# Optimization experiments

Measured on AMD Instinct MI355X. Metric: run time of the kernel, lower is better.

Reference implementation:

```python
import jax, jax.numpy as jnp
import numpy as np

B, Hs, Ws, DIM = 8, 32, 32, 768
NH, HD = 12, 64  # num_heads, head_dim


def get_rel_pos(size, rel_pos):
    # q_size == k_size == size; no interpolation branch needed
    coords = jnp.arange(size)[:, None] - jnp.arange(size)[None, :] + (size - 1)
    return rel_pos[coords]  # (size, size, head_dim)


def setup_inputs() -> dict:
    key = jax.random.key(0)
    ks = jax.random.split(key, 7)
    inv = 1.0 / np.sqrt(DIM)
    return {
        "x": jax.random.normal(ks[0], (B, Hs, Ws, DIM), jnp.float32),
        "qkv_w": jax.random.normal(ks[1], (3 * DIM, DIM), jnp.float32) * inv,
        "qkv_b": jax.random.normal(ks[2], (3 * DIM,), jnp.float32) * 0.02,
        "proj_w": jax.random.normal(ks[3], (DIM, DIM), jnp.float32) * inv,
        "proj_b": jax.random.normal(ks[4], (DIM,), jnp.float32) * 0.02,
        "rel_pos_h": jax.random.normal(ks[5], (2 * Hs - 1, HD), jnp.float32) * 0.02,
        "rel_pos_w": jax.random.normal(ks[6], (2 * Ws - 1, HD), jnp.float32) * 0.02,
    }


def reference(x, qkv_w, qkv_b, proj_w, proj_b, rel_pos_h, rel_pos_w):
    Bb, H, W, C = x.shape
    L = H * W
    scale = HD ** -0.5

    qkv = x @ qkv_w.T + qkv_b                       # (B,H,W,3C)
    qkv = qkv.reshape(Bb, L, 3, NH, HD).transpose(2, 0, 3, 1, 4)
    q, k, v = qkv[0], qkv[1], qkv[2]                # (B,NH,L,HD)

    # decomposed 2D relative position bias
    rel_h = get_rel_pos(H, rel_pos_h)               # (H,H,HD)
    rel_w = get_rel_pos(W, rel_pos_w)               # (W,W,HD)
    q5 = q.reshape(Bb, NH, H, W, HD)
    rel_h_attn = jnp.einsum('bnhwc,hkc->bnhwk', q5, rel_h)  # (B,NH,H,W,H)
    rel_w_attn = jnp.einsum('bnhwc,wkc->bnhwk', q5, rel_w)  # (B,NH,H,W,W)
    bias = rel_h_attn[..., :, None] + rel_w_attn[..., None, :]  # (B,NH,H,W,H,W)
    bias = bias.reshape(Bb, NH, L, L)

    scores = jnp.einsum('bnqd,bnkd->bnqk', q, k) * scale + bias
    attn = jax.nn.softmax(scores, axis=-1)
    out = jnp.einsum('bnqk,bnkd->bnqd', attn, v)    # (B,NH,L,HD)

    out = out.reshape(Bb, NH, H, W, HD).transpose(0, 2, 3, 1, 4).reshape(Bb, H, W, C)
    return out @ proj_w.T + proj_b
```

## Files before the change

kernel.cpp:

```cpp
#include <hip/hip_runtime.h>

typedef unsigned short u16;
typedef __bf16 bf16x8 __attribute__((ext_vector_type(8)));
typedef float f32x4 __attribute__((ext_vector_type(4)));

#define NHEAD 12
#define LQ 1024
#define HDIM 64
#define DIMM 768

__device__ __forceinline__ u16 f2b(float f) {
  unsigned u = __float_as_uint(f);
  u += 0x7fffu + ((u >> 16) & 1u);
  return (u16)(u >> 16);
}
__device__ __forceinline__ float b2f(u16 v) {
  return __uint_as_float(((unsigned)v) << 16);
}
__device__ __forceinline__ unsigned cvt_pk(float lo, float hi) {
  unsigned r;
  asm("v_cvt_pk_bf16_f32 %0, %1, %2" : "=v"(r) : "v"(lo), "v"(hi));
  return r;
}
__device__ __forceinline__ void async16(const void* g, void* l) {
  __builtin_amdgcn_global_load_lds(
      (const __attribute__((address_space(1))) void*)g,
      (__attribute__((address_space(3))) void*)l, 16, 0, 0);
}

__global__ __launch_bounds__(256) void cvt_kernel(const float* __restrict__ in,
                                                  u16* __restrict__ out, int n4) {
  int i = blockIdx.x * 256 + threadIdx.x;
  if (i >= n4) return;
  const float4 v = reinterpret_cast<const float4*>(in)[i];
  ushort4 o;
  o.x = f2b(v.x); o.y = f2b(v.y); o.z = f2b(v.z); o.w = f2b(v.w);
  reinterpret_cast<ushort4*>(out)[i] = o;
}

__global__ __launch_bounds__(256) void cvt_rel(const float* __restrict__ rph,
                                               const float* __restrict__ rpw,
                                               u16* __restrict__ rphb,
                                               u16* __restrict__ rpwb) {
  int i = blockIdx.x * 256 + threadIdx.x;
  int tab = i >> 12, idx = i & 4095;
  int m = idx >> 6, d = idx & 63;
  const float* src = tab ? rpw : rph;
  u16* dst = tab ? rpwb : rphb;
  dst[idx] = (m < 63) ? f2b(src[m * HDIM + d]) : (u16)0;
}

__global__ __launch_bounds__(256) void gemm_qkv(const u16* __restrict__ A,
                                                const u16* __restrict__ Bt,
                                                const float* __restrict__ bias,
                                                u16* __restrict__ qb,
                                                u16* __restrict__ kb,
                                                u16* __restrict__ vtb) {
  __shared__ u16 la[128 * 32];
  __shared__ u16 lb[128 * 32];
  const int K = DIMM;
  int t = threadIdx.x;
  int lane = t & 63, wv = t >> 6;
  int l15 = lane & 15, l4 = lane >> 4;
  int bm = blockIdx.x / 18, bn = blockIdx.x % 18;
  int m0 = bm * 128, n0 = bn * 128;
  int wm = (wv >> 1) * 64, wn = (wv & 1) * 64;

  f32x4 acc[4][4];
  #pragma unroll
  for (int i = 0; i < 4; ++i)
    #pragma unroll
    for (int j = 0; j < 4; ++j) acc[i][j] = {0.f, 0.f, 0.f, 0.f};

  for (int k0 = 0; k0 < K; k0 += 32) {
    __syncthreads();
    #pragma unroll
    for (int i = 0; i < 2; ++i) {
      int c = i * 256 + t;
      int row = c >> 2, co = c & 3;
      async16(A + (m0 + row) * K + k0 + co * 8, (char*)la + c * 16);
      async16(Bt + (n0 + row) * K + k0 + co * 8, (char*)lb + c * 16);
    }
    __syncthreads();
    bf16x8 af[4], bfr[4];
    #pragma unroll
    for (int mi = 0; mi < 4; ++mi)
      af[mi] = *reinterpret_cast<const bf16x8*>(&la[(wm + mi * 16 + l15) * 32 + l4 * 8]);
    #pragma unroll
    for (int nj = 0; nj < 4; ++nj)
      bfr[nj] = *reinterpret_cast<const bf16x8*>(&lb[(wn + nj * 16 + l15) * 32 + l4 * 8]);
    #pragma unroll
    for (int mi = 0; mi < 4; ++mi)
      #pragma unroll
      for (int nj = 0; nj < 4; ++nj)
        acc[mi][nj] = __builtin_amdgcn_mfma_f32_16x16x32_bf16(af[mi], bfr[nj], acc[mi][nj], 0, 0, 0);
  }

  int part = (n0 >> 7) / 6;
  #pragma unroll
  for (int nj = 0; nj < 4; ++nj) {
    int n = n0 + wn + nj * 16 + l15;
    float bv = bias[n];
    int d = n & 63;
    int head = (n >> 6) % NHEAD;
    #pragma unroll
    for (int mi = 0; mi < 4; ++mi) {
      #pragma unroll
      for (int r = 0; r < 4; ++r) {
        int m = m0 + wm + mi * 16 + l4 * 4 + r;
        int b = m >> 10, li = m & 1023;
        int bh = b * NHEAD + head;
        u16 o = f2b(acc[mi][nj][r] + bv);
        if (part == 0)      qb[(bh * LQ + li) * HDIM + d] = o;
        else if (part == 1) kb[(bh * LQ + li) * HDIM + d] = o;
        else                vtb[(bh * HDIM + d) * LQ + li] = o;
      }
    }
  }
}

__global__ __launch_bounds__(256) void attn_kernel(const u16* __restrict__ qb,
                                                   const u16* __restrict__ kb,
                                                   const u16* __restrict__ vtb,
                                                   const u16* __restrict__ rphb,
                                                   const u16* __restrict__ rpwb,
                                                   u16* __restrict__ ao) {
  __shared__ u16 lds_k[64 * 64];
  __shared__ u16 lds_v[64 * 64];
  __shared__ u16 lds_th[64 * 72];
  __shared__ u16 lds_tw[64 * 72];
  __shared__ u16 lds_p[4][16 * 72];

  int bid = blockIdx.x;
  int bh = bid >> 4;
  int q0 = (bid & 15) * 64;
  int t = threadIdx.x;
  int wv = t >> 6, lane = t & 63;
  int l15 = lane & 15, l4 = lane >> 4;

  bf16x8 qf[2];
  {
    const u16* qsrc = qb + (bh * LQ + q0 + wv * 16 + l15) * HDIM + l4 * 8;
    qf[0] = *reinterpret_cast<const bf16x8*>(qsrc);
    qf[1] = *reinterpret_cast<const bf16x8*>(qsrc + 32);
  }

  #pragma unroll
  for (int c = 0; c < 4; ++c) {
    f32x4 th = {0.f, 0.f, 0.f, 0.f}, tw = {0.f, 0.f, 0.f, 0.f};
    #pragma unroll
    for (int ks2 = 0; ks2 < 2; ++ks2) {
      bf16x8 bhf = *reinterpret_cast<const bf16x8*>(&rphb[(c * 16 + l15) * HDIM + ks2 * 32 + l4 * 8]);
      bf16x8 bwf = *reinterpret_cast<const bf16x8*>(&rpwb[(c * 16 + l15) * HDIM + ks2 * 32 + l4 * 8]);
      th = __builtin_amdgcn_mfma_f32_16x16x32_bf16(qf[ks2], bhf, th, 0, 0, 0);
      tw = __builtin_amdgcn_mfma_f32_16x16x32_bf16(qf[ks2], bwf, tw, 0, 0, 0);
    }
    #pragma unroll
    for (int r = 0; r < 4; ++r) {
      int row = wv * 16 + l4 * 4 + r;
      lds_th[row * 72 + c * 16 + l15] = f2b(th[r]);
      lds_tw[row * 72 + c * 16 + l15] = f2b(tw[r]);
    }
  }

  int gq = q0 + wv * 16 + l15;
  int hq = gq >> 5, wq = gq & 31;
  int lrow = wv * 16 + l15;
  const u16* thp = &lds_th[lrow * 72 + hq + 31];
  const u16* twp = &lds_tw[lrow * 72 + wq + 31];

  float m_run = -1e30f, l_run = 0.f;
  f32x4 acc_o[4];
  #pragma unroll
  for (int dj = 0; dj < 4; ++dj) acc_o[dj] = {0.f, 0.f, 0.f, 0.f};

  u16* pl = &lds_p[wv][0];

  for (int kv0 = 0; kv0 < LQ; kv0 += 64) {
    __syncthreads();
    {
      const u16* ks = kb + (bh * LQ + kv0) * HDIM;
      const u16* vs = vtb + bh * HDIM * LQ + kv0;
      #pragma unroll
      for (int i = 0; i < 2; ++i) {
        int c = i * 256 + t;
        int row = c >> 3, co = c & 7;
        int g = co ^ (row & 7);
        async16(ks + row * HDIM + g * 8, (char*)lds_k + c * 16);
        async16(vs + row * LQ + g * 8, (char*)lds_v + c * 16);
      }
    }
    __syncthreads();

    f32x4 sc[4];
    #pragma unroll
    for (int nj = 0; nj < 4; ++nj) {
      f32x4 a = {0.f, 0.f, 0.f, 0.f};
      #pragma unroll
      for (int ks2 = 0; ks2 < 2; ++ks2) {
        int co = (ks2 * 4 + l4) ^ (l15 & 7);
        bf16x8 kf = *reinterpret_cast<const bf16x8*>(&lds_k[(nj * 16 + l15) * 64 + co * 8]);
        a = __builtin_amdgcn_mfma_f32_16x16x32_bf16(kf, qf[ks2], a, 0, 0, 0);
      }
      sc[nj] = a;
    }

    int kv5 = kv0 >> 5;
    float th0 = b2f(thp[-kv5]);
    float th1 = b2f(thp[-kv5 - 1]);
    float p[4][4];
    float cmax = -1e30f;
    #pragma unroll
    for (int nj = 0; nj < 4; ++nj) {
      float thv = (nj < 2) ? th0 : th1;
      int kb2 = (nj & 1) * 16 + l4 * 4;
      #pragma unroll
      for (int r = 0; r < 4; ++r) {
        float s = fmaf(sc[nj][r], 0.125f, thv) + b2f(twp[-(kb2 + r)]);
        p[nj][r] = s;
        cmax = fmaxf(cmax, s);
      }
    }
    cmax = fmaxf(cmax, __shfl_xor(cmax, 16));
    cmax = fmaxf(cmax, __shfl_xor(cmax, 32));

    if (!__all(cmax <= m_run + 8.0f)) {
      float mn = fmaxf(m_run, cmax);
      float scl = __expf(m_run - mn);
      m_run = mn;
      l_run *= scl;
      #pragma unroll
      for (int dj = 0; dj < 4; ++dj)
        #pragma unroll
        for (int r = 0; r < 4; ++r) acc_o[dj][r] *= scl;
    }

    float psum = 0.f;
    #pragma unroll
    for (int nj = 0; nj < 4; ++nj)
      #pragma unroll
      for (int r = 0; r < 4; ++r) {
        p[nj][r] = __expf(p[nj][r] - m_run);
        psum += p[nj][r];
      }
    psum += __shfl_xor(psum, 16);
    psum += __shfl_xor(psum, 32);
    l_run += psum;

    #pragma unroll
    for (int nj = 0; nj < 4; ++nj) {
      uint2 pk;
      pk.x = cvt_pk(p[nj][0], p[nj][1]);
      pk.y = cvt_pk(p[nj][2], p[nj][3]);
      *reinterpret_cast<uint2*>(&pl[l15 * 72 + nj * 16 + l4 * 4]) = pk;
    }

    bf16x8 pf[2];
    pf[0] = *reinterpret_cast<const bf16x8*>(&pl[l15 * 72 + l4 * 8]);
    pf[1] = *reinterpret_cast<const bf16x8*>(&pl[l15 * 72 + 32 + l4 * 8]);

    #pragma unroll
    for (int dj = 0; dj < 4; ++dj) {
      int d = dj * 16 + l15;
      #pragma unroll
      for (int ks2 = 0; ks2 < 2; ++ks2) {
        int co = (ks2 * 4 + l4) ^ (l15 & 7);
        bf16x8 vf = *reinterpret_cast<const bf16x8*>(&lds_v[d * 64 + co * 8]);
        acc_o[dj] = __builtin_amdgcn_mfma_f32_16x16x32_bf16(vf, pf[ks2], acc_o[dj], 0, 0, 0);
      }
    }
  }

  int b = bh / NHEAD, head = bh % NHEAD;
  float inv = 1.f / l_run;
  u16* orow = ao + (b * LQ + gq) * DIMM + head * HDIM;
  #pragma unroll
  for (int dj = 0; dj < 4; ++dj) {
    uint2 pk;
    pk.x = cvt_pk(acc_o[dj][0] * inv, acc_o[dj][1] * inv);
    pk.y = cvt_pk(acc_o[dj][2] * inv, acc_o[dj][3] * inv);
    *reinterpret_cast<uint2*>(&orow[dj * 16 + l4 * 4]) = pk;
  }
}

__global__ __launch_bounds__(256) void gemm_proj(const u16* __restrict__ A,
                                                 const u16* __restrict__ Bt,
                                                 const float* __restrict__ bias,
                                                 float* __restrict__ out) {
  __shared__ u16 la[128 * 32];
  __shared__ u16 lb[128 * 32];
  const int K = DIMM;
  int t = threadIdx.x;
  int lane = t & 63, wv = t >> 6;
  int l15 = lane & 15, l4 = lane >> 4;
  int bm = blockIdx.x / 6, bn = blockIdx.x % 6;
  int m0 = bm * 128, n0 = bn * 128;
  int wm = (wv >> 1) * 64, wn = (wv & 1) * 64;

  f32x4 acc[4][4];
  #pragma unroll
  for (int i = 0; i < 4; ++i)
    #pragma unroll
    for (int j = 0; j < 4; ++j) acc[i][j] = {0.f, 0.f, 0.f, 0.f};

  for (int k0 = 0; k0 < K; k0 += 32) {
    __syncthreads();
    #pragma unroll
    for (int i = 0; i < 2; ++i) {
      int c = i * 256 + t;
      int row = c >> 2, co = c & 3;
      async16(A + (m0 + row) * K + k0 + co * 8, (char*)la + c * 16);
      async16(Bt + (n0 + row) * K + k0 + co * 8, (char*)lb + c * 16);
    }
    __syncthreads();
    bf16x8 af[4], bfr[4];
    #pragma unroll
    for (int mi = 0; mi < 4; ++mi)
      af[mi] = *reinterpret_cast<const bf16x8*>(&la[(wm + mi * 16 + l15) * 32 + l4 * 8]);
    #pragma unroll
    for (int nj = 0; nj < 4; ++nj)
      bfr[nj] = *reinterpret_cast<const bf16x8*>(&lb[(wn + nj * 16 + l15) * 32 + l4 * 8]);
    #pragma unroll
    for (int mi = 0; mi < 4; ++mi)
      #pragma unroll
      for (int nj = 0; nj < 4; ++nj)
        acc[mi][nj] = __builtin_amdgcn_mfma_f32_16x16x32_bf16(af[mi], bfr[nj], acc[mi][nj], 0, 0, 0);
  }

  #pragma unroll
  for (int nj = 0; nj < 4; ++nj) {
    int n = n0 + wn + nj * 16 + l15;
    float bv = bias[n];
    #pragma unroll
    for (int mi = 0; mi < 4; ++mi) {
      #pragma unroll
      for (int r = 0; r < 4; ++r) {
        int m = m0 + wm + mi * 16 + l4 * 4 + r;
        out[m * DIMM + n] = acc[mi][nj][r] + bv;
      }
    }
  }
}

extern "C" void kernel_launch(void* const* d_in, const int* in_sizes, int n_in,
                              void* d_out, int out_size, void* d_ws, size_t ws_size,
                              hipStream_t stream) {
  const float* x      = (const float*)d_in[0];
  const float* qkv_w  = (const float*)d_in[1];
  const float* qkv_b  = (const float*)d_in[2];
  const float* proj_w = (const float*)d_in[3];
  const float* proj_b = (const float*)d_in[4];
  const float* rph    = (const float*)d_in[5];
  const float* rpw    = (const float*)d_in[6];
  float* out = (float*)d_out;
  char* ws = (char*)d_ws;

  u16*   xb     = (u16*)(ws + 0);
  u16*   wqkvb  = (u16*)(ws + 12582912);
  u16*   wprojb = (u16*)(ws + 16121856);
  u16*   qb     = (u16*)(ws + 17301504);
  u16*   kb     = (u16*)(ws + 29884416);
  u16*   vtb    = (u16*)(ws + 42467328);
  u16*   rphb   = (u16*)(ws + 55050240);
  u16*   rpwb   = (u16*)(ws + 55058432);
  u16*   ao     = xb;

  cvt_kernel<<<6144, 256, 0, stream>>>(x, xb, 8192 * 768 / 4);
  cvt_kernel<<<1728, 256, 0, stream>>>(qkv_w, wqkvb, 2304 * 768 / 4);
  cvt_kernel<<<576, 256, 0, stream>>>(proj_w, wprojb, 768 * 768 / 4);
  cvt_rel<<<32, 256, 0, stream>>>(rph, rpw, rphb, rpwb);

  gemm_qkv<<<64 * 18, 256, 0, stream>>>(xb, wqkvb, qkv_b, qb, kb, vtb);

  attn_kernel<<<96 * 16, 256, 0, stream>>>(qb, kb, vtb, rphb, rpwb, ao);

  gemm_proj<<<64 * 6, 256, 0, stream>>>(ao, wprojb, proj_b, out);
}
```

Before: 186.7 us.

## Double-buffer LDS tiles, swizzle block order, and raise MFMA wave priority

The QKV and projection GEMMs and the attention K/V loop now use two LDS buffers. The next tile's async global-to-LDS loads are issued right after the top barrier, so they overlap with the current tile's MFMA work. A raw barrier at the end of each iteration stops a buffer from being overwritten while still being read. Block indices are remapped in strides of eight, presumably to group neighbouring tiles per XCD for better L2 reuse. The attention MFMA sections are wrapped in s_setprio to favour matrix issue. The cost is double the LDS footprint for the staged tiles, which may reduce occupancy.

Result: slower. 206.2 us (+10.5%).

```diff
diff --git a/kernel.cpp b/kernel.cpp
--- a/kernel.cpp
+++ b/kernel.cpp
@@ -26,6 +26,11 @@
   __builtin_amdgcn_global_load_lds(
       (const __attribute__((address_space(1))) void*)g,
       (__attribute__((address_space(3))) void*)l, 16, 0, 0);
+}
+__device__ __forceinline__ void raw_barrier() {
+  asm volatile("s_waitcnt lgkmcnt(0)" ::: "memory");
+  __builtin_amdgcn_sched_barrier(0);
+  __builtin_amdgcn_s_barrier();
 }
 
 __global__ __launch_bounds__(256) void cvt_kernel(const float* __restrict__ in,
@@ -56,44 +61,53 @@
                                                 u16* __restrict__ qb,
                                                 u16* __restrict__ kb,
                                                 u16* __restrict__ vtb) {
-  __shared__ u16 la[128 * 32];
-  __shared__ u16 lb[128 * 32];
+  __shared__ u16 la[2][128 * 32];
+  __shared__ u16 lb[2][128 * 32];
   const int K = DIMM;
   int t = threadIdx.x;
   int lane = t & 63, wv = t >> 6;
   int l15 = lane & 15, l4 = lane >> 4;
-  int bm = blockIdx.x / 18, bn = blockIdx.x % 18;
+  int swz = (blockIdx.x & 7) * 144 + (blockIdx.x >> 3);
+  int bm = swz / 18, bn = swz % 18;
   int m0 = bm * 128, n0 = bn * 128;
   int wm = (wv >> 1) * 64, wn = (wv & 1) * 64;
 
-  f32x4 acc[4][4];
-  #pragma unroll
-  for (int i = 0; i < 4; ++i)
-    #pragma unroll
-    for (int j = 0; j < 4; ++j) acc[i][j] = {0.f, 0.f, 0.f, 0.f};
-
-  for (int k0 = 0; k0 < K; k0 += 32) {
-    __syncthreads();
+  auto stage = [&](int s, int buf) {
+    int k0 = s * 32;
     #pragma unroll
     for (int i = 0; i < 2; ++i) {
       int c = i * 256 + t;
       int row = c >> 2, co = c & 3;
-      async16(A + (m0 + row) * K + k0 + co * 8, (char*)la + c * 16);
-      async16(Bt + (n0 + row) * K + k0 + co * 8, (char*)lb + c * 16);
-    }
+      async16(A + (m0 + row) * K + k0 + co * 8, (char*)&la[buf][0] + c * 16);
+      async16(Bt + (n0 + row) * K + k0 + co * 8, (char*)&lb[buf][0] + c * 16);
+    }
+  };
+
+  f32x4 acc[4][4];
+  #pragma unroll
+  for (int i = 0; i < 4; ++i)
+    #pragma unroll
+    for (int j = 0; j < 4; ++j) acc[i][j] = {0.f, 0.f, 0.f, 0.f};
+
+  stage(0, 0);
+  #pragma unroll 2
+  for (int s = 0; s < 24; ++s) {
+    int cur = s & 1;
     __syncthreads();
+    if (s + 1 < 24) stage(s + 1, cur ^ 1);
     bf16x8 af[4], bfr[4];
     #pragma unroll
     for (int mi = 0; mi < 4; ++mi)
-      af[mi] = *reinterpret_cast<const bf16x8*>(&la[(wm + mi * 16 + l15) * 32 + l4 * 8]);
+      af[mi] = *reinterpret_cast<const bf16x8*>(&la[cur][(wm + mi * 16 + l15) * 32 + l4 * 8]);
     #pragma unroll
     for (int nj = 0; nj < 4; ++nj)
-      bfr[nj] = *reinterpret_cast<const bf16x8*>(&lb[(wn + nj * 16 + l15) * 32 + l4 * 8]);
+      bfr[nj] = *reinterpret_cast<const bf16x8*>(&lb[cur][(wn + nj * 16 + l15) * 32 + l4 * 8]);
     #pragma unroll
     for (int mi = 0; mi < 4; ++mi)
       #pragma unroll
       for (int nj = 0; nj < 4; ++nj)
         acc[mi][nj] = __builtin_amdgcn_mfma_f32_16x16x32_bf16(af[mi], bfr[nj], acc[mi][nj], 0, 0, 0);
+    raw_barrier();
   }
 
   int part = (n0 >> 7) / 6;
@@ -125,18 +139,33 @@
                                                    const u16* __restrict__ rphb,
                                                    const u16* __restrict__ rpwb,
                                                    u16* __restrict__ ao) {
-  __shared__ u16 lds_k[64 * 64];
-  __shared__ u16 lds_v[64 * 64];
+  __shared__ u16 lds_k[2][64 * 64];
+  __shared__ u16 lds_v[2][64 * 64];
   __shared__ u16 lds_th[64 * 72];
   __shared__ u16 lds_tw[64 * 72];
   __shared__ u16 lds_p[4][16 * 72];
 
-  int bid = blockIdx.x;
-  int bh = bid >> 4;
-  int q0 = (bid & 15) * 64;
+  int swz = (blockIdx.x & 7) * 192 + (blockIdx.x >> 3);
+  int bh = swz >> 4;
+  int q0 = (swz & 15) * 64;
   int t = threadIdx.x;
   int wv = t >> 6, lane = t & 63;
   int l15 = lane & 15, l4 = lane >> 4;
+
+  auto stagekv = [&](int kv0, int buf) {
+    const u16* ks = kb + (bh * LQ + kv0) * HDIM;
+    const u16* vs = vtb + bh * HDIM * LQ + kv0;
+    #pragma unroll
+    for (int i = 0; i < 2; ++i) {
+      int c = i * 256 + t;
+      int row = c >> 3, co = c & 7;
+      int g = co ^ (row & 7);
+      async16(ks + row * HDIM + g * 8, (char*)&lds_k[buf][0] + c * 16);
+      async16(vs + row * LQ + g * 8, (char*)&lds_v[buf][0] + c * 16);
+    }
+  };
+
+  stagekv(0, 0);
 
   bf16x8 qf[2];
   {
@@ -176,34 +205,27 @@
 
   u16* pl = &lds_p[wv][0];
 
-  for (int kv0 = 0; kv0 < LQ; kv0 += 64) {
+  #pragma unroll 2
+  for (int cidx = 0; cidx < 16; ++cidx) {
+    int cur = cidx & 1;
+    int kv0 = cidx * 64;
     __syncthreads();
-    {
-      const u16* ks = kb + (bh * LQ + kv0) * HDIM;
-      const u16* vs = vtb + bh * HDIM * LQ + kv0;
-      #pragma unroll
-      for (int i = 0; i < 2; ++i) {
-        int c = i * 256 + t;
-        int row = c >> 3, co = c & 7;
-        int g = co ^ (row & 7);
-        async16(ks + row * HDIM + g * 8, (char*)lds_k + c * 16);
-        async16(vs + row * LQ + g * 8, (char*)lds_v + c * 16);
-      }
-    }
-    __syncthreads();
+    if (cidx + 1 < 16) stagekv(kv0 + 64, cur ^ 1);
 
     f32x4 sc[4];
+    __builtin_amdgcn_s_setprio(1);
     #pragma unroll
     for (int nj = 0; nj < 4; ++nj) {
       f32x4 a = {0.f, 0.f, 0.f, 0.f};
       #pragma unroll
       for (int ks2 = 0; ks2 < 2; ++ks2) {
         int co = (ks2 * 4 + l4) ^ (l15 & 7);
-        bf16x8 kf = *reinterpret_cast<const bf16x8*>(&lds_k[(nj * 16 + l15) * 64 + co * 8]);
+        bf16x8 kf = *reinterpret_cast<const bf16x8*>(&lds_k[cur][(nj * 16 + l15) * 64 + co * 8]);
         a = __builtin_amdgcn_mfma_f32_16x16x32_bf16(kf, qf[ks2], a, 0, 0, 0);
       }
       sc[nj] = a;
     }
+    __builtin_amdgcn_s_setprio(0);
 
     int kv5 = kv0 >> 5;
     float th0 = b2f(thp[-kv5]);
@@ -259,16 +281,20 @@
     pf[0] = *reinterpret_cast<const bf16x8*>(&pl[l15 * 72 + l4 * 8]);
     pf[1] = *reinterpret_cast<const bf16x8*>(&pl[l15 * 72 + 32 + l4 * 8]);
 
+    __builtin_amdgcn_s_setprio(1);
     #pragma unroll
     for (int dj = 0; dj < 4; ++dj) {
       int d = dj * 16 + l15;
       #pragma unroll
       for (int ks2 = 0; ks2 < 2; ++ks2) {
         int co = (ks2 * 4 + l4) ^ (l15 & 7);
-        bf16x8 vf = *reinterpret_cast<const bf16x8*>(&lds_v[d * 64 + co * 8]);
+        bf16x8 vf = *reinterpret_cast<const bf16x8*>(&lds_v[cur][d * 64 + co * 8]);
         acc_o[dj] = __builtin_amdgcn_mfma_f32_16x16x32_bf16(vf, pf[ks2], acc_o[dj], 0, 0, 0);
       }
     }
+    __builtin_amdgcn_s_setprio(0);
+
+    raw_barrier();
   }
 
   int b = bh / NHEAD, head = bh % NHEAD;
@@ -287,44 +313,53 @@
                                                  const u16* __restrict__ Bt,
                                                  const float* __restrict__ bias,
                                                  float* __restrict__ out) {
-  __shared__ u16 la[128 * 32];
-  __shared__ u16 lb[128 * 32];
+  __shared__ u16 la[2][128 * 32];
+  __shared__ u16 lb[2][128 * 32];
   const int K = DIMM;
   int t = threadIdx.x;
   int lane = t & 63, wv = t >> 6;
   int l15 = lane & 15, l4 = lane >> 4;
-  int bm = blockIdx.x / 6, bn = blockIdx.x % 6;
+  int swz = (blockIdx.x & 7) * 48 + (blockIdx.x >> 3);
+  int bm = swz / 6, bn = swz % 6;
   int m0 = bm * 128, n0 = bn * 128;
   int wm = (wv >> 1) * 64, wn = (wv & 1) * 64;
 
-  f32x4 acc[4][4];
-  #pragma unroll
-  for (int i = 0; i < 4; ++i)
-    #pragma unroll
-    for (int j = 0; j < 4; ++j) acc[i][j] = {0.f, 0.f, 0.f, 0.f};
-
-  for (int k0 = 0; k0 < K; k0 += 32) {
-    __syncthreads();
+  auto stage = [&](int s, int buf) {
+    int k0 = s * 32;
     #pragma unroll
     for (int i = 0; i < 2; ++i) {
       int c = i * 256 + t;
       int row = c >> 2, co = c & 3;
-      async16(A + (m0 + row) * K + k0 + co * 8, (char*)la + c * 16);
-      async16(Bt + (n0 + row) * K + k0 + co * 8, (char*)lb + c * 16);
-    }
+      async16(A + (m0 + row) * K + k0 + co * 8, (char*)&la[buf][0] + c * 16);
+      async16(Bt + (n0 + row) * K + k0 + co * 8, (char*)&lb[buf][0] + c * 16);
+    }
+  };
+
+  f32x4 acc[4][4];
+  #pragma unroll
+  for (int i = 0; i < 4; ++i)
+    #pragma unroll
+    for (int j = 0; j < 4; ++j) acc[i][j] = {0.f, 0.f, 0.f, 0.f};
+
+  stage(0, 0);
+  #pragma unroll 2
+  for (int s = 0; s < 24; ++s) {
+    int cur = s & 1;
     __syncthreads();
+    if (s + 1 < 24) stage(s + 1, cur ^ 1);
     bf16x8 af[4], bfr[4];
     #pragma unroll
     for (int mi = 0; mi < 4; ++mi)
-      af[mi] = *reinterpret_cast<const bf16x8*>(&la[(wm + mi * 16 + l15) * 32 + l4 * 8]);
+      af[mi] = *reinterpret_cast<const bf16x8*>(&la[cur][(wm + mi * 16 + l15) * 32 + l4 * 8]);
     #pragma unroll
     for (int nj = 0; nj < 4; ++nj)
-      bfr[nj] = *reinterpret_cast<const bf16x8*>(&lb[(wn + nj * 16 + l15) * 32 + l4 * 8]);
+      bfr[nj] = *reinterpret_cast<const bf16x8*>(&lb[cur][(wn + nj * 16 + l15) * 32 + l4 * 8]);
     #pragma unroll
     for (int mi = 0; mi < 4; ++mi)
       #pragma unroll
       for (int nj = 0; nj < 4; ++nj)
         acc[mi][nj] = __builtin_amdgcn_mfma_f32_16x16x32_bf16(af[mi], bfr[nj], acc[mi][nj], 0, 0, 0);
+    raw_barrier();
   }
 
   #pragma unroll
```
